# Optimization experiments

Measured on AMD Instinct MI355X. Metric: run time of the kernel, lower is better.

## Reference

```python
import jax, jax.numpy as jnp
import numpy as np

B, C, H, W = 8, 256, 64, 64
CR = C // 8  # reduced channels = 32


def setup_inputs() -> dict:
    key = jax.random.key(0)
    k1, k2, k3, k4 = jax.random.split(key, 4)
    x = jax.random.normal(k1, (B, C, H, W), dtype=jnp.float32)
    # 1x1 conv weights (bias=False) are plain channel matmuls; scale like kaiming (~1/sqrt(fan_in))
    Wt = jax.random.normal(k2, (3 * CR, C), dtype=jnp.float32) * (1.0 / np.sqrt(C))
    Wo = jax.random.normal(k3, (C, CR), dtype=jnp.float32) * (1.0 / np.sqrt(CR))
    scale = jax.random.normal(k4, (1,), dtype=jnp.float32)
    return {"x": x, "Wt": Wt, "Wo": Wo, "scale": scale}


def reference(x, Wt, Wo, scale):
    b, c, h, w = x.shape
    n = h * w
    # 1x1 conv QKV projection: [B, 3*Cr, H, W]
    t = jnp.einsum('oc,bchw->bohw', Wt, x)
    cr = t.shape[1] // 3
    key = t[:, :cr].reshape(b, cr, n)          # [B, Cr, N]
    query = t[:, cr:2 * cr].reshape(b, cr, n)  # [B, Cr, N]
    value = t[:, 2 * cr:].reshape(b, cr, n)    # [B, Cr, N]
    # scores[b, i, j] = sum_c key[b,c,i] * query[b,c,j]  (key^T @ query)
    scores = jnp.einsum('bci,bcj->bij', key, query)  # [B, N, N]
    # torch Softmax(dim=1): normalize over the key axis i
    weights = jax.nn.softmax(scores, axis=1)
    # output[b, c, j] = sum_i value[b,c,i] * weights[b,i,j]
    out = jnp.einsum('bci,bij->bcj', value, weights)  # [B, Cr, N]
    out = out.reshape(b, cr, h, w)
    out = jnp.einsum('oc,bchw->bohw', Wo, out)  # 1x1 conv back to C channels
    return scale[0] * out + x
```

## Files before the change

kernel.cpp:

```cpp
#include <hip/hip_runtime.h>
#include <math.h>

#define B_ 8
#define C_ 256
#define CR_ 32
#define N_ 4096
#define NH_ 8

typedef __attribute__((ext_vector_type(8))) short bf16x8;
typedef __attribute__((ext_vector_type(4))) short bf16x4;
typedef __attribute__((ext_vector_type(4))) float f32x4;
typedef __attribute__((ext_vector_type(16))) float f32x16;
typedef __attribute__((ext_vector_type(2))) unsigned uint32x2;

#if defined(__has_builtin)
#if __has_builtin(__builtin_amdgcn_permlane32_swap)
#define HAVE_PLSWAP 1
#endif
#endif

__device__ inline short f2bf(float f) {
  union { float f; unsigned u; } v; v.f = f;
  unsigned r = v.u + 0x7FFFu + ((v.u >> 16) & 1u);
  return (short)(r >> 16);
}
__device__ inline float bf2f(short h) {
  union { unsigned u; float f; } v; v.u = ((unsigned)(unsigned short)h) << 16;
  return v.f;
}
__device__ inline short f2bf_r(float f) {
  return (short)((__float_as_uint(f) + 0x8000u) >> 16);
}

__device__ inline unsigned cvt_pk_bf16(float a, float b) {
  unsigned d;
  asm("v_cvt_pk_bf16_f32 %0, %1, %2" : "=v"(d) : "v"(a), "v"(b));
  return d;
}


__global__ __launch_bounds__(256) void prep_weights(const float* __restrict__ Wt,
                                                    const float* __restrict__ Wo,
                                                    const float* __restrict__ scale,
                                                    short* __restrict__ WtHi,
                                                    short* __restrict__ WtLo,
                                                    short* __restrict__ WoB) {
  const int blk = blockIdx.x, tid = threadIdx.x;
  if (blk < 96) {
    float v = Wt[blk * C_ + tid];
    if (blk >= 32 && blk < 64) v *= 1.44269504f;
    const short h = f2bf(v);
    WtHi[blk * C_ + tid] = h;
    WtLo[blk * C_ + tid] = f2bf(v - bf2f(h));
  } else {
    const int idx = (blk - 96) * 256 + tid;
    WoB[idx] = f2bf(Wo[idx] * scale[0]);
  }
}

__global__ __launch_bounds__(256) void qkv_mfma(const float* __restrict__ x,
                                                const short* __restrict__ WtHi,
                                                const short* __restrict__ WtLo,
                                                short* __restrict__ Kf,
                                                short* __restrict__ Qf,
                                                short* __restrict__ Vf) {
  const int b = blockIdx.y;
  const int tid = threadIdx.x;
  const int wave = tid >> 6, lane = tid & 63;
  const int col = lane & 15, quad = lane >> 4;
  const int n0 = (blockIdx.x * 4 + wave) * 16;

  const f32x4 z4 = {0.f, 0.f, 0.f, 0.f};
  f32x4 acc[6] = {z4, z4, z4, z4, z4, z4};

  const float* xb = x + (size_t)b * C_ * N_ + n0 + col;
  float xcur[8], xnxt[8];
#pragma unroll
  for (int j = 0; j < 8; ++j) xcur[j] = xb[(size_t)(quad * 8 + j) * N_];

#pragma unroll 2
  for (int c0 = 0; c0 < C_; c0 += 32) {
    if (c0 < C_ - 32) {
#pragma unroll
      for (int j = 0; j < 8; ++j)
        xnxt[j] = xb[(size_t)(c0 + 32 + quad * 8 + j) * N_];
    }
    bf16x8 xh, xl;
#pragma unroll
    for (int j = 0; j < 8; ++j) {
      const short h = (short)(__float_as_uint(xcur[j]) >> 16);
      xh[j] = h;
      xl[j] = f2bf_r(xcur[j] - bf2f(h));
    }
#pragma unroll
    for (int ot = 0; ot < 4; ++ot) {
      const int off = (ot * 16 + col) * C_ + c0 + quad * 8;
      const bf16x8 bh = *(const bf16x8*)(WtHi + off);
      const bf16x8 bl = *(const bf16x8*)(WtLo + off);
      acc[ot] = __builtin_amdgcn_mfma_f32_16x16x32_bf16(xh, bh, acc[ot], 0, 0, 0);
      acc[ot] = __builtin_amdgcn_mfma_f32_16x16x32_bf16(xl, bh, acc[ot], 0, 0, 0);
      acc[ot] = __builtin_amdgcn_mfma_f32_16x16x32_bf16(xh, bl, acc[ot], 0, 0, 0);
    }
#pragma unroll
    for (int ct = 0; ct < 2; ++ct) {
      const int off = ((64 + ct * 16) + col) * C_ + c0 + quad * 8;
      const bf16x8 ah = *(const bf16x8*)(WtHi + off);
      const bf16x8 al = *(const bf16x8*)(WtLo + off);
      acc[4 + ct] = __builtin_amdgcn_mfma_f32_16x16x32_bf16(ah, xh, acc[4 + ct], 0, 0, 0);
      acc[4 + ct] = __builtin_amdgcn_mfma_f32_16x16x32_bf16(ah, xl, acc[4 + ct], 0, 0, 0);
      acc[4 + ct] = __builtin_amdgcn_mfma_f32_16x16x32_bf16(al, xh, acc[4 + ct], 0, 0, 0);
    }
#pragma unroll
    for (int j = 0; j < 8; ++j) xcur[j] = xnxt[j];
  }

#pragma unroll
  for (int ot = 0; ot < 2; ++ot)
#pragma unroll
    for (int r = 0; r < 4; ++r) {
      const int i = n0 + quad * 4 + r;
      const int c = ot * 16 + col;
      const int ln = (i & 31) | (((c >> 3) & 1) << 5);
      Kf[(((size_t)(b * 128 + (i >> 5)) * 2 + (c >> 4)) * 64 + ln) * 8 + (c & 7)] =
          f2bf(acc[ot][r]);
    }
#pragma unroll
  for (int ot = 2; ot < 4; ++ot)
#pragma unroll
    for (int r = 0; r < 4; ++r) {
      const int j = n0 + quad * 4 + r;
      const int c = (ot - 2) * 16 + col;
      const int ln = (j & 31) | (((c >> 3) & 1) << 5);
      Qf[(((size_t)(b * 128 + (j >> 5)) * 2 + (c >> 4)) * 64 + ln) * 8 + (c & 7)] =
          f2bf(acc[ot][r]);
    }
#pragma unroll
  for (int ct = 0; ct < 2; ++ct)
#pragma unroll
    for (int r = 0; r < 4; ++r) {
      const int c = ct * 16 + quad * 4 + r;
      const int n = n0 + col;
      const int ln = c | (((n >> 3) & 1) << 5);
      Vf[((size_t)(b * 256 + (n >> 4)) * 64 + ln) * 8 + (n & 7)] =
          f2bf(acc[4 + ct][r]);
    }
}

__global__ __launch_bounds__(128) void flash_attn(const short* __restrict__ Kf,
                                                  const short* __restrict__ Qf,
                                                  const short* __restrict__ Vf,
                                                  short* __restrict__ OPart,
                                                  float* __restrict__ LPart) {
  const int b = blockIdx.z, hq = blockIdx.y;
  const int tid = threadIdx.x;
  const int jt = blockIdx.x * 2 + (tid >> 6);
  const int lane = tid & 63;
  const int j32 = lane & 31, h32 = lane >> 5;

  const f32x16 z16 = {0.f};
  const short* pQ = Qf + ((size_t)(b * 128 + jt) * 2) * 512 + lane * 8;
  const bf16x8 qf0 = *(const bf16x8*)(pQ);
  const bf16x8 qf1 = *(const bf16x8*)(pQ + 512);

  const short* pK = Kf + ((size_t)(b * 128 + hq * 16) * 2) * 512 + lane * 8;
  const short* pV = Vf + ((size_t)(b * 256 + hq * 32)) * 512 + lane * 8;

  f32x16 acc = z16;
  float ps = 0.f;

  bf16x8 ka = *(const bf16x8*)(pK);
  bf16x8 kb = *(const bf16x8*)(pK + 512);

#pragma unroll 1
  for (int t = 0; t < 16; ++t) {
    const bf16x8 va = *(const bf16x8*)(pV);
    const bf16x8 vb = *(const bf16x8*)(pV + 512);
    pK += 1024;
    pV += 1024;
    const bf16x8 kan = *(const bf16x8*)(pK);
    const bf16x8 kbn = *(const bf16x8*)(pK + 512);

    __builtin_amdgcn_s_setprio(1);
    f32x16 s = __builtin_amdgcn_mfma_f32_32x32x16_bf16(ka, qf0, z16, 0, 0, 0);
    s = __builtin_amdgcn_mfma_f32_32x32x16_bf16(kb, qf1, s, 0, 0, 0);
    __builtin_amdgcn_s_setprio(0);
    float p[16];
#pragma unroll
    for (int r = 0; r < 16; ++r) p[r] = __builtin_amdgcn_exp2f(s[r]);
    ps += (((p[0] + p[1]) + (p[2] + p[3])) + ((p[4] + p[5]) + (p[6] + p[7]))) +
          (((p[8] + p[9]) + (p[10] + p[11])) + ((p[12] + p[13]) + (p[14] + p[15])));
    union { unsigned u[4]; bf16x8 v; } f0, f1;
#ifdef HAVE_PLSWAP
    {
      const unsigned d0 = cvt_pk_bf16(p[0], p[1]);
      const unsigned d1 = cvt_pk_bf16(p[2], p[3]);
      const unsigned d2 = cvt_pk_bf16(p[4], p[5]);
      const unsigned d3 = cvt_pk_bf16(p[6], p[7]);
      const uint32x2 r0 = __builtin_amdgcn_permlane32_swap(d0, d2, false, false);
      f0.u[0] = r0[0]; f0.u[2] = r0[1];
      const uint32x2 r1 = __builtin_amdgcn_permlane32_swap(d1, d3, false, false);
      f0.u[1] = r1[0]; f0.u[3] = r1[1];
      const unsigned d4 = cvt_pk_bf16(p[8], p[9]);
      const unsigned d5 = cvt_pk_bf16(p[10], p[11]);
      const unsigned d6 = cvt_pk_bf16(p[12], p[13]);
      const unsigned d7 = cvt_pk_bf16(p[14], p[15]);
      const uint32x2 r2 = __builtin_amdgcn_permlane32_swap(d4, d6, false, false);
      f1.u[0] = r2[0]; f1.u[2] = r2[1];
      const uint32x2 r3 = __builtin_amdgcn_permlane32_swap(d5, d7, false, false);
      f1.u[1] = r3[0]; f1.u[3] = r3[1];
    }
#else
    {
      unsigned d[8], xw[8];
#pragma unroll
      for (int k = 0; k < 8; ++k) d[k] = cvt_pk_bf16(p[2 * k], p[2 * k + 1]);
#pragma unroll
      for (int k = 0; k < 8; ++k) xw[k] = __shfl_xor((int)d[k], 32);
      f0.u[0] = h32 ? xw[2] : d[0];
      f0.u[1] = h32 ? xw[3] : d[1];
      f0.u[2] = h32 ? d[2] : xw[0];
      f0.u[3] = h32 ? d[3] : xw[1];
      f1.u[0] = h32 ? xw[6] : d[4];
      f1.u[1] = h32 ? xw[7] : d[5];
      f1.u[2] = h32 ? d[6] : xw[4];
      f1.u[3] = h32 ? d[7] : xw[5];
    }
#endif
    __builtin_amdgcn_s_setprio(1);
    acc = __builtin_amdgcn_mfma_f32_32x32x16_bf16(va, f0.v, acc, 0, 0, 0);
    acc = __builtin_amdgcn_mfma_f32_32x32x16_bf16(vb, f1.v, acc, 0, 0, 0);
    __builtin_amdgcn_s_setprio(0);

    ka = kan;
    kb = kbn;
  }

  const size_t base = ((size_t)b * NH_ + hq) * N_;
  const float l = ps + __shfl_xor(ps, 32);
  const int jg = jt * 32 + j32;
  if (h32 == 0) LPart[base + jg] = l;
  short* OP = OPart + (base + jg) * 32;
#pragma unroll
  for (int g = 0; g < 4; ++g) {
    bf16x4 o = {f2bf(acc[4 * g + 0]), f2bf(acc[4 * g + 1]),
                f2bf(acc[4 * g + 2]), f2bf(acc[4 * g + 3])};
    *(bf16x4*)(OP + 8 * g + 4 * h32) = o;
  }
}

__global__ __launch_bounds__(256) void out_proj(const short* __restrict__ OPart,
                                                const float* __restrict__ LPart,
                                                const short* __restrict__ WoB,
                                                const float* __restrict__ x,
                                                float* __restrict__ out) {
  const int b = blockIdx.z, chalf = blockIdx.y;
  const int tid = threadIdx.x;
  const int wave = tid >> 6, lane = tid & 63;
  const int col = lane & 15, quad = lane >> 4;
  const int jg = blockIdx.x * 64 + wave * 16 + col;
  const int n0 = blockIdx.x * 64 + wave * 16;

  float osum[8];
#pragma unroll
  for (int e = 0; e < 8; ++e) osum[e] = 0.f;
  float lsum = 0.f;
#pragma unroll
  for (int h = 0; h < NH_; ++h) {
    const size_t p = ((size_t)b * NH_ + h) * N_ + jg;
    const bf16x8 o = *(const bf16x8*)(OPart + p * 32 + quad * 8);
#pragma unroll
    for (int e = 0; e < 8; ++e) osum[e] += bf2f(o[e]);
    lsum += LPart[p];
  }
  const float linv = 1.f / lsum;
  bf16x8 bf;
#pragma unroll
  for (int e = 0; e < 8; ++e) bf[e] = f2bf(osum[e] * linv);

  const f32x4 z4 = {0.f, 0.f, 0.f, 0.f};
  const float* xb = x + (size_t)b * C_ * N_;
  float* ob = out + (size_t)b * C_ * N_;
#pragma unroll
  for (int ct = 0; ct < 8; ++ct) {
    const int ctg = chalf * 8 + ct;
    const bf16x8 af = *(const bf16x8*)(WoB + (ctg * 16 + col) * 32 + quad * 8);
    const f32x4 a = __builtin_amdgcn_mfma_f32_16x16x32_bf16(af, bf, z4, 0, 0, 0);
#pragma unroll
    for (int r = 0; r < 4; ++r) {
      const size_t idx = (size_t)(ctg * 16 + quad * 4 + r) * N_ + n0 + col;
      ob[idx] = a[r] + xb[idx];
    }
  }
}

extern "C" void kernel_launch(void* const* d_in, const int* in_sizes, int n_in,
                              void* d_out, int out_size, void* d_ws,
                              size_t ws_size, hipStream_t stream) {
  const float* x = (const float*)d_in[0];
  const float* Wt = (const float*)d_in[1];
  const float* Wo = (const float*)d_in[2];
  const float* scale = (const float*)d_in[3];
  float* out = (float*)d_out;

  short* OPart = (short*)d_ws;
  float* LPart = (float*)(OPart + (size_t)B_ * NH_ * N_ * 32);
  short* Kf = (short*)(LPart + (size_t)B_ * NH_ * N_);
  short* Qf = Kf + (size_t)B_ * 128 * 1024;
  short* Vf = Qf + (size_t)B_ * 128 * 1024;
  short* WtHi = Vf + (size_t)B_ * 256 * 512;
  short* WtLo = WtHi + 96 * C_;
  short* WoB = WtLo + 96 * C_;

  prep_weights<<<dim3(128), 256, 0, stream>>>(Wt, Wo, scale, WtHi, WtLo, WoB);
  qkv_mfma<<<dim3(64, B_), 256, 0, stream>>>(x, WtHi, WtLo, Kf, Qf, Vf);
  flash_attn<<<dim3(64, NH_, B_), 128, 0, stream>>>(Kf, Qf, Vf, OPart, LPart);
  out_proj<<<dim3(64, 2, B_), 256, 0, stream>>>(OPart, LPart, WoB, x, out);
}
```

Baseline: 156.2 us.

## Stage K/V chunk in LDS shared by 8 waves and remap blocks per XCD

The flash attention kernel now runs 512-thread blocks of 8 waves. Each block cooperatively loads its 512-key K and V chunk into shared memory once, and every wave then reads it from LDS instead of from global memory. Block IDs are remapped so that the blocks sharing a (batch, head-chunk) group land on the same XCD, which should improve L2 locality. The trade-offs are 64KB of LDS per block, which limits occupancy, an upfront load followed by a barrier with no overlap, and larger blocks.

New measurement: 150.7 us. 3.5% less time.

```diff
diff --git a/kernel.cpp b/kernel.cpp
--- a/kernel.cpp
+++ b/kernel.cpp
@@ -146,39 +146,58 @@
     }
 }
 
-__global__ __launch_bounds__(128) void flash_attn(const short* __restrict__ Kf,
+__global__ __launch_bounds__(512) void flash_attn(const short* __restrict__ Kf,
                                                   const short* __restrict__ Qf,
                                                   const short* __restrict__ Vf,
                                                   short* __restrict__ OPart,
                                                   float* __restrict__ LPart) {
-  const int b = blockIdx.z, hq = blockIdx.y;
+  __shared__ short Ks[16384];
+  __shared__ short Vs[16384];
+
+  const int bid = blockIdx.x;
+  const int xcd = bid & 7, w = bid >> 3;
+  const int g = xcd * 8 + (w >> 4);
+  const int b = g >> 3, hq = g & 7;
+  const int jp = w & 15;
   const int tid = threadIdx.x;
-  const int jt = blockIdx.x * 2 + (tid >> 6);
-  const int lane = tid & 63;
+  const int wave = tid >> 6, lane = tid & 63;
+  const int jt = jp * 8 + wave;
   const int j32 = lane & 31, h32 = lane >> 5;
+
+  {
+    const bf16x8* gK = (const bf16x8*)(Kf + ((size_t)(b * 128 + hq * 16) * 2) * 512);
+    const bf16x8* gV = (const bf16x8*)(Vf + ((size_t)(b * 256 + hq * 32)) * 512);
+    bf16x8* sK = (bf16x8*)Ks;
+    bf16x8* sV = (bf16x8*)Vs;
+#pragma unroll
+    for (int i = 0; i < 4; ++i) {
+      sK[tid + i * 512] = gK[tid + i * 512];
+      sV[tid + i * 512] = gV[tid + i * 512];
+    }
+  }
+  __syncthreads();
 
   const f32x16 z16 = {0.f};
   const short* pQ = Qf + ((size_t)(b * 128 + jt) * 2) * 512 + lane * 8;
   const bf16x8 qf0 = *(const bf16x8*)(pQ);
   const bf16x8 qf1 = *(const bf16x8*)(pQ + 512);
 
-  const short* pK = Kf + ((size_t)(b * 128 + hq * 16) * 2) * 512 + lane * 8;
-  const short* pV = Vf + ((size_t)(b * 256 + hq * 32)) * 512 + lane * 8;
-
   f32x16 acc = z16;
   float ps = 0.f;
 
-  bf16x8 ka = *(const bf16x8*)(pK);
-  bf16x8 kb = *(const bf16x8*)(pK + 512);
+  const short* sKl = Ks + lane * 8;
+  const short* sVl = Vs + lane * 8;
+
+  bf16x8 ka = *(const bf16x8*)(sKl);
+  bf16x8 kb = *(const bf16x8*)(sKl + 512);
 
 #pragma unroll 1
   for (int t = 0; t < 16; ++t) {
-    const bf16x8 va = *(const bf16x8*)(pV);
-    const bf16x8 vb = *(const bf16x8*)(pV + 512);
-    pK += 1024;
-    pV += 1024;
-    const bf16x8 kan = *(const bf16x8*)(pK);
-    const bf16x8 kbn = *(const bf16x8*)(pK + 512);
+    const bf16x8 va = *(const bf16x8*)(sVl + t * 1024);
+    const bf16x8 vb = *(const bf16x8*)(sVl + t * 1024 + 512);
+    const int tn = (t + 1) & 15;
+    const bf16x8 kan = *(const bf16x8*)(sKl + tn * 1024);
+    const bf16x8 kbn = *(const bf16x8*)(sKl + tn * 1024 + 512);
 
     __builtin_amdgcn_s_setprio(1);
     f32x16 s = __builtin_amdgcn_mfma_f32_32x32x16_bf16(ka, qf0, z16, 0, 0, 0);
@@ -241,10 +260,10 @@
   if (h32 == 0) LPart[base + jg] = l;
   short* OP = OPart + (base + jg) * 32;
 #pragma unroll
-  for (int g = 0; g < 4; ++g) {
-    bf16x4 o = {f2bf(acc[4 * g + 0]), f2bf(acc[4 * g + 1]),
-                f2bf(acc[4 * g + 2]), f2bf(acc[4 * g + 3])};
-    *(bf16x4*)(OP + 8 * g + 4 * h32) = o;
+  for (int g2 = 0; g2 < 4; ++g2) {
+    bf16x4 o = {f2bf(acc[4 * g2 + 0]), f2bf(acc[4 * g2 + 1]),
+                f2bf(acc[4 * g2 + 2]), f2bf(acc[4 * g2 + 3])};
+    *(bf16x4*)(OP + 8 * g2 + 4 * h32) = o;
   }
 }
 
@@ -313,6 +332,6 @@
 
   prep_weights<<<dim3(128), 256, 0, stream>>>(Wt, Wo, scale, WtHi, WtLo, WoB);
   qkv_mfma<<<dim3(64, B_), 256, 0, stream>>>(x, WtHi, WtLo, Kf, Qf, Vf);
-  flash_attn<<<dim3(64, NH_, B_), 128, 0, stream>>>(Kf, Qf, Vf, OPart, LPart);
+  flash_attn<<<dim3(1024), 512, 0, stream>>>(Kf, Qf, Vf, OPart, LPart);
   out_proj<<<dim3(64, 2, B_), 256, 0, stream>>>(OPart, LPart, WoB, x, out);
 }
```
